# Kernel tuning notes

Measured on AMD Instinct MI355X. Metric: run time of the kernel, lower is better.

## Reference

```python
import jax, jax.numpy as jnp
import numpy as np

N, E = 50000, 800000
D_IN, D_HID, D_OUT = 128, 64, 32
NEG_SLOPE = 0.2


def _gat_layer(h_in, src, dst, W, a_s, a_d, b):
    # h_in: [N, din], W: [din, dout]
    h = h_in @ W                                   # [N, dout]
    alpha_src = h @ a_s                            # [N]
    alpha_dst = h @ a_d                            # [N]
    e = jax.nn.leaky_relu(alpha_src[src] + alpha_dst[dst], NEG_SLOPE)  # [E']
    # segment softmax over incoming edges of each dst node
    m = jax.ops.segment_max(e, dst, num_segments=N)
    ex = jnp.exp(e - m[dst])
    s = jax.ops.segment_sum(ex, dst, num_segments=N)
    w = ex / s[dst]                                # [E']
    out = jax.ops.segment_sum(h[src] * w[:, None], dst, num_segments=N)
    return out + b


def setup_inputs() -> dict:
    key = jax.random.key(0)
    ks = jax.random.split(key, 16)
    x = jax.random.normal(ks[0], (N, D_IN), dtype=jnp.float32)
    edge_index = jax.random.randint(ks[1], (2, E), 0, N, dtype=jnp.int64)
    dims = [(D_IN, D_HID), (D_HID, D_HID), (D_HID, D_OUT)]
    inp = {"x": x, "edge_index": edge_index}
    for i, (din, dout) in enumerate(dims):
        sc = 1.0 / np.sqrt(din)
        inp[f"W{i}"] = jax.random.normal(ks[2 + 4 * i], (din, dout), dtype=jnp.float32) * sc
        inp[f"as{i}"] = jax.random.normal(ks[3 + 4 * i], (dout,), dtype=jnp.float32) * 0.1
        inp[f"ad{i}"] = jax.random.normal(ks[4 + 4 * i], (dout,), dtype=jnp.float32) * 0.1
        inp[f"b{i}"] = jnp.zeros((dout,), dtype=jnp.float32)
    return inp


def reference(x, edge_index, W0, as0, ad0, b0, W1, as1, ad1, b1, W2, as2, ad2, b2):
    # add self loops (PyG GATConv default)
    loop = jnp.arange(N, dtype=edge_index.dtype)
    src = jnp.concatenate([edge_index[0], loop])
    dst = jnp.concatenate([edge_index[1], loop])
    h = jax.nn.relu(_gat_layer(x, src, dst, W0, as0, ad0, b0))
    h = jax.nn.relu(_gat_layer(h, src, dst, W1, as1, ad1, b1))
    h = jnp.tanh(_gat_layer(h, src, dst, W2, as2, ad2, b2))
    return h
```

## Files before the change

### kernel.cpp

```cpp
#include <hip/hip_runtime.h>
#include <hip/hip_fp16.h>
#include <math.h>

#define N_NODES 50000
#define E_EDGES 800000
#define ETOT    (E_EDGES + N_NODES)

#define BUCK_SHIFT 9
#define BUCK_SZ   (1 << BUCK_SHIFT)
#define NBUCK ((N_NODES + BUCK_SZ - 1) >> BUCK_SHIFT)
#define BS_EPT 16
#define BS_THREADS 256
#define BS_EPB (BS_THREADS * BS_EPT)
#define BS_NBLK ((ETOT + BS_EPB - 1) / BS_EPB)

template<int DIN, int DOUT>
__global__ __launch_bounds__(256)
void gemm_alpha_kernel(const float* __restrict__ X, const float* __restrict__ W,
                       const float* __restrict__ a_s, const float* __restrict__ a_d,
                       __half* __restrict__ H16, float* __restrict__ asrc,
                       float* __restrict__ adst)
{
    constexpr int COLG = DOUT / 4;
    constexpr int ROWG = 256 / COLG;
    constexpr int BM   = ROWG * 4;
    constexpr int K4   = DIN / 4;

    __shared__ float Xl[BM * DIN];
    __shared__ float Wl[DIN * DOUT];

    const int tid = threadIdx.x;
    const int row0b = blockIdx.x * BM;

    constexpr int WV = DIN * DOUT / 4;
    for (int i = tid; i < WV; i += 256)
        ((float4*)Wl)[i] = ((const float4*)W)[i];

    constexpr int XV = BM * K4;
    for (int i = tid; i < XV; i += 256) {
        int r  = i / K4;
        int j  = i % K4;
        int gr = row0b + r;
        float4 v = make_float4(0.f, 0.f, 0.f, 0.f);
        if (gr < N_NODES) v = ((const float4*)X)[gr * K4 + j];
        *(float4*)&Xl[r * DIN + ((j ^ ((r >> 2) & 7)) << 2)] = v;
    }
    __syncthreads();

    const int tx = tid % COLG;
    const int ty = tid / COLG;
    const int r0 = ty * 4;
    const int c0 = tx * 4;
    const int swz = ty & 7;

    float acc[4][4] = {};
    for (int kk = 0; kk < DIN; kk += 4) {
        float a[4][4], w[4][4];
        const int jk = ((kk >> 2) ^ swz) << 2;
#pragma unroll
        for (int i = 0; i < 4; ++i)
            *(float4*)a[i] = *(const float4*)&Xl[(r0 + i) * DIN + jk];
#pragma unroll
        for (int j = 0; j < 4; ++j)
            *(float4*)w[j] = *(const float4*)&Wl[(kk + j) * DOUT + c0];
#pragma unroll
        for (int i = 0; i < 4; ++i)
#pragma unroll
            for (int j = 0; j < 4; ++j)
                acc[i][j] = fmaf(a[i][0], w[0][j],
                            fmaf(a[i][1], w[1][j],
                            fmaf(a[i][2], w[2][j],
                            fmaf(a[i][3], w[3][j], acc[i][j]))));
    }

    float as4[4], ad4[4];
    *(float4*)as4 = *(const float4*)&a_s[c0];
    *(float4*)ad4 = *(const float4*)&a_d[c0];

#pragma unroll
    for (int i = 0; i < 4; ++i) {
        const int gr = row0b + r0 + i;
        float ps = acc[i][0] * as4[0] + acc[i][1] * as4[1] +
                   acc[i][2] * as4[2] + acc[i][3] * as4[3];
        float pd = acc[i][0] * ad4[0] + acc[i][1] * ad4[1] +
                   acc[i][2] * ad4[2] + acc[i][3] * ad4[3];
#pragma unroll
        for (int off = COLG / 2; off >= 1; off >>= 1) {
            ps += __shfl_xor(ps, off, 64);
            pd += __shfl_xor(pd, off, 64);
        }
        if (gr < N_NODES) {
            __half2 p01 = __floats2half2_rn(acc[i][0], acc[i][1]);
            __half2 p23 = __floats2half2_rn(acc[i][2], acc[i][3]);
            uint2 pk;
            pk.x = *(unsigned int*)&p01;
            pk.y = *(unsigned int*)&p23;
            *(uint2*)&H16[gr * DOUT + c0] = pk;
            if (tx == 0) { asrc[gr] = ps; adst[gr] = pd; }
        }
    }
}

__global__ __launch_bounds__(128)
void zero98_kernel(int* __restrict__ bcnt)
{
    int i = threadIdx.x;
    if (i < NBUCK) bcnt[i] = 0;
}

__global__ __launch_bounds__(BS_THREADS)
void hist_kernel(const int* __restrict__ ei, int* __restrict__ bcnt)
{
    __shared__ int lcnt[NBUCK];
    const int t = threadIdx.x;
    for (int i = t; i < NBUCK; i += BS_THREADS) lcnt[i] = 0;
    __syncthreads();
    const int e0 = blockIdx.x * BS_EPB;
#pragma unroll
    for (int k = 0; k < BS_EPT; ++k) {
        const int eid = e0 + k * BS_THREADS + t;
        if (eid < ETOT) {
            int dst = (eid < E_EDGES) ? ei[E_EDGES + eid] : (eid - E_EDGES);
            atomicAdd(&lcnt[dst >> BUCK_SHIFT], 1);
        }
    }
    __syncthreads();
    for (int i = t; i < NBUCK; i += BS_THREADS)
        if (lcnt[i] > 0) atomicAdd(&bcnt[i], lcnt[i]);
}

__global__ __launch_bounds__(128)
void scan98_kernel(const int* __restrict__ bcnt, int* __restrict__ cur,
                   int* __restrict__ cur0)
{
    __shared__ int lds[128];
    const int t = threadIdx.x;
    const int v = (t < NBUCK) ? bcnt[t] : 0;
    lds[t] = v;
    __syncthreads();
    for (int off = 1; off < 128; off <<= 1) {
        int u = (t >= off) ? lds[t - off] : 0;
        __syncthreads();
        lds[t] += u;
        __syncthreads();
    }
    if (t < NBUCK) { cur[t] = lds[t] - v; cur0[t] = lds[t] - v; }
}

__global__ __launch_bounds__(BS_THREADS)
void binscatter_kernel(const int* __restrict__ ei, int* __restrict__ cur,
                       unsigned int* __restrict__ tmp)
{
    __shared__ int lcnt[NBUCK];
    __shared__ int lbase[NBUCK];
    const int t = threadIdx.x;
    for (int i = t; i < NBUCK; i += BS_THREADS) lcnt[i] = 0;
    __syncthreads();

    const int e0 = blockIdx.x * BS_EPB;
    unsigned int pk[BS_EPT];
    int rk[BS_EPT];
    int bk[BS_EPT];
#pragma unroll
    for (int k = 0; k < BS_EPT; ++k) {
        const int eid = e0 + k * BS_THREADS + t;
        bk[k] = -1;
        if (eid < ETOT) {
            int src, dst;
            if (eid < E_EDGES) { src = ei[eid]; dst = ei[E_EDGES + eid]; }
            else               { src = dst = eid - E_EDGES; }
            bk[k] = dst >> BUCK_SHIFT;
            pk[k] = ((unsigned int)dst << 16) | (unsigned int)src;
            rk[k] = atomicAdd(&lcnt[bk[k]], 1);
        }
    }
    __syncthreads();
    for (int i = t; i < NBUCK; i += BS_THREADS)
        if (lcnt[i] > 0) lbase[i] = atomicAdd(&cur[i], lcnt[i]);
    __syncthreads();
#pragma unroll
    for (int k = 0; k < BS_EPT; ++k)
        if (bk[k] >= 0) tmp[lbase[bk[k]] + rk[k]] = pk[k];
}

__global__ __launch_bounds__(BUCK_SZ)
void bucket_sort_kernel(const unsigned int* __restrict__ tmp,
                        const int* __restrict__ cur0,
                        const int* __restrict__ bcnt,
                        unsigned int* __restrict__ csr_pk,
                        int* __restrict__ offs)
{
    __shared__ int lcnt[BUCK_SZ];
    __shared__ int loff[BUCK_SZ];
    __shared__ int lcur[BUCK_SZ];
    const int bk = blockIdx.x;
    const int t  = threadIdx.x;
    const int base = cur0[bk];
    const int cnt  = bcnt[bk];

    lcnt[t] = 0;
    __syncthreads();
    for (int i = t; i < cnt; i += BUCK_SZ)
        atomicAdd(&lcnt[(tmp[base + i] >> 16) & (BUCK_SZ - 1)], 1);
    __syncthreads();

    const int v = lcnt[t];
    loff[t] = v;
    __syncthreads();
    for (int off = 1; off < BUCK_SZ; off <<= 1) {
        int u = (t >= off) ? loff[t - off] : 0;
        __syncthreads();
        loff[t] += u;
        __syncthreads();
    }
    const int excl = loff[t] - v;

    const int g = (bk << BUCK_SHIFT) + t;
    if (g <= N_NODES) offs[g] = base + excl;

    lcur[t] = excl;
    __syncthreads();
    for (int i = t; i < cnt; i += BUCK_SZ) {
        const unsigned int pk = tmp[base + i];
        const int l = (pk >> 16) & (BUCK_SZ - 1);
        const int pos = atomicAdd(&lcur[l], 1);
        csr_pk[base + pos] = pk;
    }
}

template<int DOUT, int ACT>
__global__ __launch_bounds__(256)
void node_agg_kernel(const int* __restrict__ offs,
                     const unsigned int* __restrict__ csr_pk,
                     const float* __restrict__ asrc,
                     const float* __restrict__ adst,
                     const __half* __restrict__ H16,
                     const float* __restrict__ b,
                     float* __restrict__ out)
{
    constexpr int FL    = DOUT / 8;
    constexpr int SLOTS = 64 / FL;
    const int wv   = threadIdx.x >> 6;
    const int lane = threadIdx.x & 63;
    const int fl   = lane % FL;
    const int slot = lane / FL;
    const int node = blockIdx.x * 4 + wv;
    if (node >= N_NODES) return;

    const int beg = offs[node];
    const int end = offs[node + 1];
    const float adn = adst[node];
    const __half* __restrict__ Hf = H16 + fl * 8;

    float s = 0.f;
    float acc[8] = {};

    int eid = beg + slot;
    bool valid = (eid < end);
    unsigned int pk = valid ? csr_pk[eid] : 0u;

    for (int cb = beg; cb < end; cb += SLOTS) {
        const int nid = cb + SLOTS + slot;
        const bool nvalid = (nid < end);
        const unsigned int npk = nvalid ? csr_pk[nid] : 0u;

        float p = 0.f;
        uint4 h = make_uint4(0u, 0u, 0u, 0u);
        if (valid) {
            const unsigned int src = pk & 0xffffu;
            float v = asrc[src] + adn;
            v = fmaxf(v, 0.2f * v);
            p = __expf(fminf(v, 80.f));
            h = *(const uint4*)(Hf + src * DOUT);
        }
        const float2 f0 = __half22float2(*(const __half2*)&h.x);
        const float2 f1 = __half22float2(*(const __half2*)&h.y);
        const float2 f2 = __half22float2(*(const __half2*)&h.z);
        const float2 f3 = __half22float2(*(const __half2*)&h.w);
        s += p;
        acc[0] = fmaf(p, f0.x, acc[0]);
        acc[1] = fmaf(p, f0.y, acc[1]);
        acc[2] = fmaf(p, f1.x, acc[2]);
        acc[3] = fmaf(p, f1.y, acc[3]);
        acc[4] = fmaf(p, f2.x, acc[4]);
        acc[5] = fmaf(p, f2.y, acc[5]);
        acc[6] = fmaf(p, f3.x, acc[6]);
        acc[7] = fmaf(p, f3.y, acc[7]);
        valid = nvalid;
        pk = npk;
    }

#pragma unroll
    for (int off = FL; off < 64; off <<= 1) {
        s += __shfl_xor(s, off, 64);
#pragma unroll
        for (int j = 0; j < 8; ++j)
            acc[j] += __shfl_xor(acc[j], off, 64);
    }

    if (slot == 0) {
        const float inv = 1.f / s;
        float o[8];
#pragma unroll
        for (int j = 0; j < 8; ++j) {
            float v = acc[j] * inv + b[fl * 8 + j];
            o[j] = (ACT == 0) ? fmaxf(v, 0.f) : tanhf(v);
        }
        *(float4*)&out[node * DOUT + fl * 8]     = *(float4*)&o[0];
        *(float4*)&out[node * DOUT + fl * 8 + 4] = *(float4*)&o[4];
    }
}


template<int DIN, int DOUT, int ACT>
static void run_layer(const float* X, const float* W, const float* a_s,
                      const float* a_d, const float* b,
                      const int* offs, const unsigned int* csr_pk,
                      __half* H16, float* asrc, float* adst,
                      float* out, hipStream_t stream)
{
    constexpr int COLG = DOUT / 4;
    constexpr int BM = (256 / COLG) * 4;
    const int gemm_grid = (N_NODES + BM - 1) / BM;
    gemm_alpha_kernel<DIN, DOUT><<<gemm_grid, 256, 0, stream>>>(
        X, W, a_s, a_d, H16, asrc, adst);

    const int agg_grid = (N_NODES + 3) / 4;
    node_agg_kernel<DOUT, ACT><<<agg_grid, 256, 0, stream>>>(
        offs, csr_pk, asrc, adst, H16, b, out);
}

extern "C" void kernel_launch(void* const* d_in, const int* in_sizes, int n_in,
                              void* d_out, int out_size, void* d_ws, size_t ws_size,
                              hipStream_t stream)
{
    const float* x  = (const float*)d_in[0];
    const int*   ei = (const int*)d_in[1];
    const float* W0 = (const float*)d_in[2];
    const float* as0= (const float*)d_in[3];
    const float* ad0= (const float*)d_in[4];
    const float* b0 = (const float*)d_in[5];
    const float* W1 = (const float*)d_in[6];
    const float* as1= (const float*)d_in[7];
    const float* ad1= (const float*)d_in[8];
    const float* b1 = (const float*)d_in[9];
    const float* W2 = (const float*)d_in[10];
    const float* as2= (const float*)d_in[11];
    const float* ad2= (const float*)d_in[12];
    const float* b2 = (const float*)d_in[13];
    float* out = (float*)d_out;

    char* wsb = (char*)d_ws;
    auto take = [&](size_t bytes) {
        char* p = wsb;
        wsb += (bytes + 255) & ~size_t(255);
        return p;
    };
    __half* h16    = (__half*)take(sizeof(__half) * N_NODES * 64);
    float* buf_act = (float*)take(sizeof(float) * N_NODES * 64);
    float* asrc    = (float*)take(sizeof(float) * N_NODES);
    float* adst    = (float*)take(sizeof(float) * N_NODES);
    int*   offs    = (int*)take(sizeof(int) * (N_NODES + 1));
    int*   bcnt    = (int*)take(sizeof(int) * NBUCK);
    int*   cur     = (int*)take(sizeof(int) * NBUCK);
    int*   cur0    = (int*)take(sizeof(int) * NBUCK);
    unsigned int* csr_pk = (unsigned int*)take(sizeof(unsigned int) * ETOT);
    unsigned int* tmp = (unsigned int*)h16;

    zero98_kernel<<<1, 128, 0, stream>>>(bcnt);
    hist_kernel<<<BS_NBLK, BS_THREADS, 0, stream>>>(ei, bcnt);
    scan98_kernel<<<1, 128, 0, stream>>>(bcnt, cur, cur0);
    binscatter_kernel<<<BS_NBLK, BS_THREADS, 0, stream>>>(ei, cur, tmp);
    bucket_sort_kernel<<<NBUCK, BUCK_SZ, 0, stream>>>(tmp, cur0, bcnt,
                                                      csr_pk, offs);

    run_layer<128, 64, 0>(x, W0, as0, ad0, b0, offs, csr_pk,
                          h16, asrc, adst, buf_act, stream);
    run_layer<64, 64, 0>(buf_act, W1, as1, ad1, b1, offs, csr_pk,
                         h16, asrc, adst, buf_act, stream);
    run_layer<64, 32, 1>(buf_act, W2, as2, ad2, b2, offs, csr_pk,
                         h16, asrc, adst, out, stream);
}
```

Measured before the change: 184.6 us.

## Fuse histogram into first GEMM and aggregation into next-layer GEMM

Folds the destination-bucket histogram into the layer-0 GEMM kernel and replaces the zeroing kernel with a memset. Each layer's aggregation is fused with the following layer's GEMM and attention projection, so the activated hidden features stay in LDS and never travel through global memory as fp32. This drops several launches and the fp32 activation round trip. In exchange, the fused blocks process 64 nodes each with a fixed loop, giving fewer blocks and lower parallelism during the irregular aggregation phase, plus extra workspace for double-buffered features.

```diff
diff --git a/kernel.cpp b/kernel.cpp
--- a/kernel.cpp
+++ b/kernel.cpp
@@ -14,16 +14,19 @@
 #define BS_EPB (BS_THREADS * BS_EPT)
 #define BS_NBLK ((ETOT + BS_EPB - 1) / BS_EPB)
 
-template<int DIN, int DOUT>
+#define GEMM0_GRID ((N_NODES + 63) / 64)
+#define HPB ((ETOT + GEMM0_GRID - 1) / GEMM0_GRID)
+
 __global__ __launch_bounds__(256)
-void gemm_alpha_kernel(const float* __restrict__ X, const float* __restrict__ W,
+void gemm0_hist_kernel(const float* __restrict__ X, const float* __restrict__ W,
                        const float* __restrict__ a_s, const float* __restrict__ a_d,
+                       const int* __restrict__ ei, int* __restrict__ bcnt,
                        __half* __restrict__ H16, float* __restrict__ asrc,
                        float* __restrict__ adst)
 {
+    constexpr int DIN = 128, DOUT = 64;
     constexpr int COLG = DOUT / 4;
-    constexpr int ROWG = 256 / COLG;
-    constexpr int BM   = ROWG * 4;
+    constexpr int BM   = 64;
     constexpr int K4   = DIN / 4;
 
     __shared__ float Xl[BM * DIN];
@@ -32,12 +35,10 @@
     const int tid = threadIdx.x;
     const int row0b = blockIdx.x * BM;
 
-    constexpr int WV = DIN * DOUT / 4;
-    for (int i = tid; i < WV; i += 256)
+    for (int i = tid; i < DIN * DOUT / 4; i += 256)
         ((float4*)Wl)[i] = ((const float4*)W)[i];
 
-    constexpr int XV = BM * K4;
-    for (int i = tid; i < XV; i += 256) {
+    for (int i = tid; i < BM * K4; i += 256) {
         int r  = i / K4;
         int j  = i % K4;
         int gr = row0b + r;
@@ -99,34 +100,20 @@
             if (tx == 0) { asrc[gr] = ps; adst[gr] = pd; }
         }
     }
-}
-
-__global__ __launch_bounds__(128)
-void zero98_kernel(int* __restrict__ bcnt)
-{
-    int i = threadIdx.x;
-    if (i < NBUCK) bcnt[i] = 0;
-}
-
-__global__ __launch_bounds__(BS_THREADS)
-void hist_kernel(const int* __restrict__ ei, int* __restrict__ bcnt)
-{
-    __shared__ int lcnt[NBUCK];
-    const int t = threadIdx.x;
-    for (int i = t; i < NBUCK; i += BS_THREADS) lcnt[i] = 0;
-    __syncthreads();
-    const int e0 = blockIdx.x * BS_EPB;
-#pragma unroll
-    for (int k = 0; k < BS_EPT; ++k) {
-        const int eid = e0 + k * BS_THREADS + t;
-        if (eid < ETOT) {
-            int dst = (eid < E_EDGES) ? ei[E_EDGES + eid] : (eid - E_EDGES);
-            atomicAdd(&lcnt[dst >> BUCK_SHIFT], 1);
-        }
-    }
-    __syncthreads();
-    for (int i = t; i < NBUCK; i += BS_THREADS)
-        if (lcnt[i] > 0) atomicAdd(&bcnt[i], lcnt[i]);
+
+    __syncthreads();
+    int* lh = (int*)Xl;
+    for (int i = tid; i < NBUCK; i += 256) lh[i] = 0;
+    __syncthreads();
+    const int h0 = blockIdx.x * HPB;
+    const int hend = min(h0 + HPB, ETOT);
+    for (int eid = h0 + tid; eid < hend; eid += 256) {
+        int dst = (eid < E_EDGES) ? ei[E_EDGES + eid] : (eid - E_EDGES);
+        atomicAdd(&lh[dst >> BUCK_SHIFT], 1);
+    }
+    __syncthreads();
+    for (int i = tid; i < NBUCK; i += 256)
+        if (lh[i] > 0) atomicAdd(&bcnt[i], lh[i]);
 }
 
 __global__ __launch_bounds__(128)
@@ -225,6 +212,163 @@
         const int l = (pk >> 16) & (BUCK_SZ - 1);
         const int pos = atomicAdd(&lcur[l], 1);
         csr_pk[base + pos] = pk;
+    }
+}
+
+template<int DOUT>
+__global__ __launch_bounds__(256)
+void fused_agg_gemm_kernel(const int* __restrict__ offs,
+                           const unsigned int* __restrict__ csr_pk,
+                           const float* __restrict__ asrc_p,
+                           const float* __restrict__ adst_p,
+                           const __half* __restrict__ H16_p,
+                           const float* __restrict__ b_p,
+                           const float* __restrict__ W,
+                           const float* __restrict__ a_s,
+                           const float* __restrict__ a_d,
+                           __half* __restrict__ H16_n,
+                           float* __restrict__ asrc_n,
+                           float* __restrict__ adst_n)
+{
+    constexpr int DIN = 64;
+    constexpr int BM  = 64;
+    __shared__ float Xl[BM * DIN];
+    __shared__ float Wl[DIN * DOUT];
+
+    const int tid = threadIdx.x;
+    for (int i = tid; i < DIN * DOUT / 4; i += 256)
+        ((float4*)Wl)[i] = ((const float4*)W)[i];
+
+    const int wv   = tid >> 6;
+    const int lane = tid & 63;
+    const int fl   = lane & 7;
+    const int slot = lane >> 3;
+    const int node0 = blockIdx.x * BM;
+    const __half* __restrict__ Hf = H16_p + fl * 8;
+
+    for (int it = 0; it < 16; ++it) {
+        const int r = it * 4 + wv;
+        const int node = node0 + r;
+        float s = 0.f;
+        float acc[8] = {};
+        if (node < N_NODES) {
+            const int beg = offs[node];
+            const int end = offs[node + 1];
+            const float adn = adst_p[node];
+            int eid = beg + slot;
+            bool valid = (eid < end);
+            unsigned int pk = valid ? csr_pk[eid] : 0u;
+            for (int cb = beg; cb < end; cb += 8) {
+                const int nid = cb + 8 + slot;
+                const bool nvalid = (nid < end);
+                const unsigned int npk = nvalid ? csr_pk[nid] : 0u;
+                float p = 0.f;
+                uint4 h = make_uint4(0u, 0u, 0u, 0u);
+                if (valid) {
+                    const unsigned int src = pk & 0xffffu;
+                    float v = asrc_p[src] + adn;
+                    v = fmaxf(v, 0.2f * v);
+                    p = __expf(fminf(v, 80.f));
+                    h = *(const uint4*)(Hf + src * 64);
+                }
+                const float2 f0 = __half22float2(*(const __half2*)&h.x);
+                const float2 f1 = __half22float2(*(const __half2*)&h.y);
+                const float2 f2 = __half22float2(*(const __half2*)&h.z);
+                const float2 f3 = __half22float2(*(const __half2*)&h.w);
+                s += p;
+                acc[0] = fmaf(p, f0.x, acc[0]);
+                acc[1] = fmaf(p, f0.y, acc[1]);
+                acc[2] = fmaf(p, f1.x, acc[2]);
+                acc[3] = fmaf(p, f1.y, acc[3]);
+                acc[4] = fmaf(p, f2.x, acc[4]);
+                acc[5] = fmaf(p, f2.y, acc[5]);
+                acc[6] = fmaf(p, f3.x, acc[6]);
+                acc[7] = fmaf(p, f3.y, acc[7]);
+                valid = nvalid;
+                pk = npk;
+            }
+        }
+#pragma unroll
+        for (int off = 8; off < 64; off <<= 1) {
+            s += __shfl_xor(s, off, 64);
+#pragma unroll
+            for (int j = 0; j < 8; ++j)
+                acc[j] += __shfl_xor(acc[j], off, 64);
+        }
+        if (slot == 0) {
+            float o[8];
+            if (node < N_NODES) {
+                const float inv = 1.f / s;
+#pragma unroll
+                for (int j = 0; j < 8; ++j)
+                    o[j] = fmaxf(acc[j] * inv + b_p[fl * 8 + j], 0.f);
+            } else {
+#pragma unroll
+                for (int j = 0; j < 8; ++j) o[j] = 0.f;
+            }
+            const int sw = (r >> 2) & 7;
+            *(float4*)&Xl[r * DIN + (((fl * 2) ^ sw) << 2)] =
+                make_float4(o[0], o[1], o[2], o[3]);
+            *(float4*)&Xl[r * DIN + (((fl * 2 + 1) ^ sw) << 2)] =
+                make_float4(o[4], o[5], o[6], o[7]);
+        }
+    }
+    __syncthreads();
+
+    constexpr int COLG = DOUT / 4;
+    constexpr int ROWG = 256 / COLG;
+    constexpr int RPT  = BM / ROWG;
+    const int tx = tid % COLG;
+    const int ty = tid / COLG;
+    const int r0 = ty * RPT;
+    const int c0 = tx * 4;
+    const int swz = (r0 >> 2) & 7;
+
+    float acg[RPT][4] = {};
+    for (int kk = 0; kk < DIN; kk += 4) {
+        float a[RPT][4], w[4][4];
+        const int jk = ((kk >> 2) ^ swz) << 2;
+#pragma unroll
+        for (int i = 0; i < RPT; ++i)
+            *(float4*)a[i] = *(const float4*)&Xl[(r0 + i) * DIN + jk];
+#pragma unroll
+        for (int j = 0; j < 4; ++j)
+            *(float4*)w[j] = *(const float4*)&Wl[(kk + j) * DOUT + c0];
+#pragma unroll
+        for (int i = 0; i < RPT; ++i)
+#pragma unroll
+            for (int j = 0; j < 4; ++j)
+                acg[i][j] = fmaf(a[i][0], w[0][j],
+                            fmaf(a[i][1], w[1][j],
+                            fmaf(a[i][2], w[2][j],
+                            fmaf(a[i][3], w[3][j], acg[i][j]))));
+    }
+
+    float as4[4], ad4[4];
+    *(float4*)as4 = *(const float4*)&a_s[c0];
+    *(float4*)ad4 = *(const float4*)&a_d[c0];
+
+#pragma unroll
+    for (int i = 0; i < RPT; ++i) {
+        const int gr = node0 + r0 + i;
+        float ps = acg[i][0] * as4[0] + acg[i][1] * as4[1] +
+                   acg[i][2] * as4[2] + acg[i][3] * as4[3];
+        float pd = acg[i][0] * ad4[0] + acg[i][1] * ad4[1] +
+                   acg[i][2] * ad4[2] + acg[i][3] * ad4[3];
+#pragma unroll
+        for (int off = COLG / 2; off >= 1; off >>= 1) {
+            ps += __shfl_xor(ps, off, 64);
+            pd += __shfl_xor(pd, off, 64);
+        }
+        if (gr < N_NODES) {
+            __half2 p01 = __floats2half2_rn(acg[i][0], acg[i][1]);
+            __half2 p23 = __floats2half2_rn(acg[i][2], acg[i][3]);
+            uint2 pk;
+            pk.x = *(unsigned int*)&p01;
+            pk.y = *(unsigned int*)&p23;
+            *(uint2*)&H16_n[gr * DOUT + c0] = pk;
+            if (tx == 0) { asrc_n[gr] = ps; adst_n[gr] = pd; }
+        }
     }
 }
 
@@ -312,24 +456,6 @@
 }
 
 
-template<int DIN, int DOUT, int ACT>
-static void run_layer(const float* X, const float* W, const float* a_s,
-                      const float* a_d, const float* b,
-                      const int* offs, const unsigned int* csr_pk,
-                      __half* H16, float* asrc, float* adst,
-                      float* out, hipStream_t stream)
-{
-    constexpr int COLG = DOUT / 4;
-    constexpr int BM = (256 / COLG) * 4;
-    const int gemm_grid = (N_NODES + BM - 1) / BM;
-    gemm_alpha_kernel<DIN, DOUT><<<gemm_grid, 256, 0, stream>>>(
-        X, W, a_s, a_d, H16, asrc, adst);
-
-    const int agg_grid = (N_NODES + 3) / 4;
-    node_agg_kernel<DOUT, ACT><<<agg_grid, 256, 0, stream>>>(
-        offs, csr_pk, asrc, adst, H16, b, out);
-}
-
 extern "C" void kernel_launch(void* const* d_in, const int* in_sizes, int n_in,
                               void* d_out, int out_size, void* d_ws, size_t ws_size,
                               hipStream_t stream)
@@ -356,28 +482,38 @@
         wsb += (bytes + 255) & ~size_t(255);
         return p;
     };
-    __half* h16    = (__half*)take(sizeof(__half) * N_NODES * 64);
-    float* buf_act = (float*)take(sizeof(float) * N_NODES * 64);
-    float* asrc    = (float*)take(sizeof(float) * N_NODES);
-    float* adst    = (float*)take(sizeof(float) * N_NODES);
+    __half* h16a   = (__half*)take(sizeof(__half) * N_NODES * 64);
+    __half* h16b   = (__half*)take(sizeof(__half) * N_NODES * 64);
+    float* asrc_a  = (float*)take(sizeof(float) * N_NODES);
+    float* adst_a  = (float*)take(sizeof(float) * N_NODES);
+    float* asrc_b  = (float*)take(sizeof(float) * N_NODES);
+    float* adst_b  = (float*)take(sizeof(float) * N_NODES);
     int*   offs    = (int*)take(sizeof(int) * (N_NODES + 1));
     int*   bcnt    = (int*)take(sizeof(int) * NBUCK);
     int*   cur     = (int*)take(sizeof(int) * NBUCK);
     int*   cur0    = (int*)take(sizeof(int) * NBUCK);
+    unsigned int* tmp    = (unsigned int*)take(sizeof(unsigned int) * ETOT);
     unsigned int* csr_pk = (unsigned int*)take(sizeof(unsigned int) * ETOT);
-    unsigned int* tmp = (unsigned int*)h16;
-
-    zero98_kernel<<<1, 128, 0, stream>>>(bcnt);
-    hist_kernel<<<BS_NBLK, BS_THREADS, 0, stream>>>(ei, bcnt);
+
+    hipMemsetAsync(bcnt, 0, sizeof(int) * NBUCK, stream);
+
+    gemm0_hist_kernel<<<GEMM0_GRID, 256, 0, stream>>>(
+        x, W0, as0, ad0, ei, bcnt, h16a, asrc_a, adst_a);
+
     scan98_kernel<<<1, 128, 0, stream>>>(bcnt, cur, cur0);
     binscatter_kernel<<<BS_NBLK, BS_THREADS, 0, stream>>>(ei, cur, tmp);
     bucket_sort_kernel<<<NBUCK, BUCK_SZ, 0, stream>>>(tmp, cur0, bcnt,
                                                       csr_pk, offs);
 
-    run_layer<128, 64, 0>(x, W0, as0, ad0, b0, offs, csr_pk,
-                          h16, asrc, adst, buf_act, stream);
-    run_layer<64, 64, 0>(buf_act, W1, as1, ad1, b1, offs, csr_pk,
-                         h16, asrc, adst, buf_act, stream);
-    run_layer<64, 32, 1>(buf_act, W2, as2, ad2, b2, offs, csr_pk,
-                         h16, asrc, adst, out, stream);
-}
+    fused_agg_gemm_kernel<64><<<GEMM0_GRID, 256, 0, stream>>>(
+        offs, csr_pk, asrc_a, adst_a, h16a, b0,
+        W1, as1, ad1, h16b, asrc_b, adst_b);
+
+    fused_agg_gemm_kernel<32><<<GEMM0_GRID, 256, 0, stream>>>(
+        offs, csr_pk, asrc_b, adst_b, h16b, b1,
+        W2, as2, ad2, h16a, asrc_a, adst_a);
+
+    const int agg_grid = (N_NODES + 3) / 4;
+    node_agg_kernel<32, 1><<<agg_grid, 256, 0, stream>>>(
+        offs, csr_pk, asrc_a, adst_a, h16a, b2, out);
+}
```

New measurement: 315.5 us. +71.0%, slower.

## Fuse edge histogram into layer-0 GEMM and fold bucket scans into consumers

Applied to the files above, without the earlier changes.

The destination-bucket histogram moves into the first-layer GEMM kernel as a tail phase, so the GEMM and histogram share one launch. The separate zero and scan kernels are removed: counters are cleared with a memset, and both binscatter and bucket_sort now recompute the prefix scan of bucket counts locally. The temporary sort buffer gets its own workspace instead of aliasing h16, since h16 is now written before the sort. This cuts kernel launches and serialization at the cost of redundant per-block scans and an extra buffer.

```diff
diff --git a/kernel.cpp b/kernel.cpp
--- a/kernel.cpp
+++ b/kernel.cpp
@@ -14,16 +14,19 @@
 #define BS_EPB (BS_THREADS * BS_EPT)
 #define BS_NBLK ((ETOT + BS_EPB - 1) / BS_EPB)
 
-template<int DIN, int DOUT>
+#define GEMM0_GRID ((N_NODES + 63) / 64)
+#define HPB ((ETOT + GEMM0_GRID - 1) / GEMM0_GRID)
+
 __global__ __launch_bounds__(256)
-void gemm_alpha_kernel(const float* __restrict__ X, const float* __restrict__ W,
+void gemm0_hist_kernel(const float* __restrict__ X, const float* __restrict__ W,
                        const float* __restrict__ a_s, const float* __restrict__ a_d,
+                       const int* __restrict__ ei, int* __restrict__ bcnt,
                        __half* __restrict__ H16, float* __restrict__ asrc,
                        float* __restrict__ adst)
 {
+    constexpr int DIN = 128, DOUT = 64;
     constexpr int COLG = DOUT / 4;
-    constexpr int ROWG = 256 / COLG;
-    constexpr int BM   = ROWG * 4;
+    constexpr int BM   = 64;
     constexpr int K4   = DIN / 4;
 
     __shared__ float Xl[BM * DIN];
@@ -32,12 +35,10 @@
     const int tid = threadIdx.x;
     const int row0b = blockIdx.x * BM;
 
-    constexpr int WV = DIN * DOUT / 4;
-    for (int i = tid; i < WV; i += 256)
+    for (int i = tid; i < DIN * DOUT / 4; i += 256)
         ((float4*)Wl)[i] = ((const float4*)W)[i];
 
-    constexpr int XV = BM * K4;
-    for (int i = tid; i < XV; i += 256) {
+    for (int i = tid; i < BM * K4; i += 256) {
         int r  = i / K4;
         int j  = i % K4;
         int gr = row0b + r;
@@ -99,61 +100,131 @@
             if (tx == 0) { asrc[gr] = ps; adst[gr] = pd; }
         }
     }
-}
-
-__global__ __launch_bounds__(128)
-void zero98_kernel(int* __restrict__ bcnt)
-{
-    int i = threadIdx.x;
-    if (i < NBUCK) bcnt[i] = 0;
+
+    __syncthreads();
+    int* lh = (int*)Xl;
+    for (int i = tid; i < NBUCK; i += 256) lh[i] = 0;
+    __syncthreads();
+    const int h0 = blockIdx.x * HPB;
+    const int hend = min(h0 + HPB, ETOT);
+    for (int eid = h0 + tid; eid < hend; eid += 256) {
+        int dst = (eid < E_EDGES) ? ei[E_EDGES + eid] : (eid - E_EDGES);
+        atomicAdd(&lh[dst >> BUCK_SHIFT], 1);
+    }
+    __syncthreads();
+    for (int i = tid; i < NBUCK; i += 256)
+        if (lh[i] > 0) atomicAdd(&bcnt[i], lh[i]);
+}
+
+template<int DIN, int DOUT>
+__global__ __launch_bounds__(256)
+void gemm_alpha_kernel(const float* __restrict__ X, const float* __restrict__ W,
+                       const float* __restrict__ a_s, const float* __restrict__ a_d,
+                       __half* __restrict__ H16, float* __restrict__ asrc,
+                       float* __restrict__ adst)
+{
+    constexpr int COLG = DOUT / 4;
+    constexpr int ROWG = 256 / COLG;
+    constexpr int BM   = ROWG * 4;
+    constexpr int K4   = DIN / 4;
+
+    __shared__ float Xl[BM * DIN];
+    __shared__ float Wl[DIN * DOUT];
+
+    const int tid = threadIdx.x;
+    const int row0b = blockIdx.x * BM;
+
+    for (int i = tid; i < DIN * DOUT / 4; i += 256)
+        ((float4*)Wl)[i] = ((const float4*)W)[i];
+
+    for (int i = tid; i < BM * K4; i += 256) {
+        int r  = i / K4;
+        int j  = i % K4;
+        int gr = row0b + r;
+        float4 v = make_float4(0.f, 0.f, 0.f, 0.f);
+        if (gr < N_NODES) v = ((const float4*)X)[gr * K4 + j];
+        *(float4*)&Xl[r * DIN + ((j ^ ((r >> 2) & 7)) << 2)] = v;
+    }
+    __syncthreads();
+
+    const int tx = tid % COLG;
+    const int ty = tid / COLG;
+    const int r0 = ty * 4;
+    const int c0 = tx * 4;
+    const int swz = ty & 7;
+
+    float acc[4][4] = {};
+    for (int kk = 0; kk < DIN; kk += 4) {
+        float a[4][4], w[4][4];
+        const int jk = ((kk >> 2) ^ swz) << 2;
+#pragma unroll
+        for (int i = 0; i < 4; ++i)
+            *(float4*)a[i] = *(const float4*)&Xl[(r0 + i) * DIN + jk];
+#pragma unroll
+        for (int j = 0; j < 4; ++j)
+            *(float4*)w[j] = *(const float4*)&Wl[(kk + j) * DOUT + c0];
+#pragma unroll
+        for (int i = 0; i < 4; ++i)
+#pragma unroll
+            for (int j = 0; j < 4; ++j)
+                acc[i][j] = fmaf(a[i][0], w[0][j],
+                            fmaf(a[i][1], w[1][j],
+                            fmaf(a[i][2], w[2][j],
+                            fmaf(a[i][3], w[3][j], acc[i][j]))));
+    }
+
+    float as4[4], ad4[4];
+    *(float4*)as4 = *(const float4*)&a_s[c0];
+    *(float4*)ad4 = *(const float4*)&a_d[c0];
+
+#pragma unroll
+    for (int i = 0; i < 4; ++i) {
+        const int gr = row0b + r0 + i;
+        float ps = acc[i][0] * as4[0] + acc[i][1] * as4[1] +
+                   acc[i][2] * as4[2] + acc[i][3] * as4[3];
+        float pd = acc[i][0] * ad4[0] + acc[i][1] * ad4[1] +
+                   acc[i][2] * ad4[2] + acc[i][3] * ad4[3];
+#pragma unroll
+        for (int off = COLG / 2; off >= 1; off >>= 1) {
+            ps += __shfl_xor(ps, off, 64);
+            pd += __shfl_xor(pd, off, 64);
+        }
+        if (gr < N_NODES) {
+            __half2 p01 = __floats2half2_rn(acc[i][0], acc[i][1]);
+            __half2 p23 = __floats2half2_rn(acc[i][2], acc[i][3]);
+            uint2 pk;
+            pk.x = *(unsigned int*)&p01;
+            pk.y = *(unsigned int*)&p23;
+            *(uint2*)&H16[gr * DOUT + c0] = pk;
+            if (tx == 0) { asrc[gr] = ps; adst[gr] = pd; }
+        }
+    }
 }
 
 __global__ __launch_bounds__(BS_THREADS)
-void hist_kernel(const int* __restrict__ ei, int* __restrict__ bcnt)
-{
-    __shared__ int lcnt[NBUCK];
-    const int t = threadIdx.x;
-    for (int i = t; i < NBUCK; i += BS_THREADS) lcnt[i] = 0;
-    __syncthreads();
-    const int e0 = blockIdx.x * BS_EPB;
-#pragma unroll
-    for (int k = 0; k < BS_EPT; ++k) {
-        const int eid = e0 + k * BS_THREADS + t;
-        if (eid < ETOT) {
-            int dst = (eid < E_EDGES) ? ei[E_EDGES + eid] : (eid - E_EDGES);
-            atomicAdd(&lcnt[dst >> BUCK_SHIFT], 1);
-        }
-    }
-    __syncthreads();
-    for (int i = t; i < NBUCK; i += BS_THREADS)
-        if (lcnt[i] > 0) atomicAdd(&bcnt[i], lcnt[i]);
-}
-
-__global__ __launch_bounds__(128)
-void scan98_kernel(const int* __restrict__ bcnt, int* __restrict__ cur,
-                   int* __restrict__ cur0)
-{
-    __shared__ int lds[128];
-    const int t = threadIdx.x;
-    const int v = (t < NBUCK) ? bcnt[t] : 0;
-    lds[t] = v;
-    __syncthreads();
-    for (int off = 1; off < 128; off <<= 1) {
-        int u = (t >= off) ? lds[t - off] : 0;
-        __syncthreads();
-        lds[t] += u;
-        __syncthreads();
-    }
-    if (t < NBUCK) { cur[t] = lds[t] - v; cur0[t] = lds[t] - v; }
-}
-
-__global__ __launch_bounds__(BS_THREADS)
-void binscatter_kernel(const int* __restrict__ ei, int* __restrict__ cur,
-                       unsigned int* __restrict__ tmp)
+void binscatter_kernel(const int* __restrict__ ei, const int* __restrict__ bcnt,
+                       int* __restrict__ cur, unsigned int* __restrict__ tmp)
 {
     __shared__ int lcnt[NBUCK];
     __shared__ int lbase[NBUCK];
+    __shared__ int lscan[128];
     const int t = threadIdx.x;
+
+    if (t < 128) {
+        const int v = (t < NBUCK) ? bcnt[t] : 0;
+        lscan[t] = v;
+        __syncthreads();
+        for (int off = 1; off < 128; off <<= 1) {
+            int u = (t >= off) ? lscan[t - off] : 0;
+            __syncthreads();
+            lscan[t] += u;
+            __syncthreads();
+        }
+        if (t < NBUCK) lbase[t] = lscan[t] - v;
+    } else {
+        __syncthreads();
+        for (int off = 1; off < 128; off <<= 1) { __syncthreads(); __syncthreads(); }
+    }
     for (int i = t; i < NBUCK; i += BS_THREADS) lcnt[i] = 0;
     __syncthreads();
 
@@ -176,7 +247,7 @@
     }
     __syncthreads();
     for (int i = t; i < NBUCK; i += BS_THREADS)
-        if (lcnt[i] > 0) lbase[i] = atomicAdd(&cur[i], lcnt[i]);
+        if (lcnt[i] > 0) lbase[i] += atomicAdd(&cur[i], lcnt[i]);
     __syncthreads();
 #pragma unroll
     for (int k = 0; k < BS_EPT; ++k)
@@ -185,7 +256,6 @@
 
 __global__ __launch_bounds__(BUCK_SZ)
 void bucket_sort_kernel(const unsigned int* __restrict__ tmp,
-                        const int* __restrict__ cur0,
                         const int* __restrict__ bcnt,
                         unsigned int* __restrict__ csr_pk,
                         int* __restrict__ offs)
@@ -193,9 +263,24 @@
     __shared__ int lcnt[BUCK_SZ];
     __shared__ int loff[BUCK_SZ];
     __shared__ int lcur[BUCK_SZ];
+    __shared__ int sbase;
     const int bk = blockIdx.x;
     const int t  = threadIdx.x;
-    const int base = cur0[bk];
+
+    {
+        const int v = (t < NBUCK) ? bcnt[t] : 0;
+        lcnt[t] = v;
+        __syncthreads();
+        for (int off = 1; off < 128; off <<= 1) {
+            int u = (t >= off && t < 128) ? lcnt[t - off] : 0;
+            __syncthreads();
+            if (t < 128) lcnt[t] += u;
+            __syncthreads();
+        }
+        if (t == bk) sbase = lcnt[t] - v;
+    }
+    __syncthreads();
+    const int base = sbase;
     const int cnt  = bcnt[bk];
 
     lcnt[t] = 0;
@@ -312,24 +397,6 @@
 }
 
 
-template<int DIN, int DOUT, int ACT>
-static void run_layer(const float* X, const float* W, const float* a_s,
-                      const float* a_d, const float* b,
-                      const int* offs, const unsigned int* csr_pk,
-                      __half* H16, float* asrc, float* adst,
-                      float* out, hipStream_t stream)
-{
-    constexpr int COLG = DOUT / 4;
-    constexpr int BM = (256 / COLG) * 4;
-    const int gemm_grid = (N_NODES + BM - 1) / BM;
-    gemm_alpha_kernel<DIN, DOUT><<<gemm_grid, 256, 0, stream>>>(
-        X, W, a_s, a_d, H16, asrc, adst);
-
-    const int agg_grid = (N_NODES + 3) / 4;
-    node_agg_kernel<DOUT, ACT><<<agg_grid, 256, 0, stream>>>(
-        offs, csr_pk, asrc, adst, H16, b, out);
-}
-
 extern "C" void kernel_launch(void* const* d_in, const int* in_sizes, int n_in,
                               void* d_out, int out_size, void* d_ws, size_t ws_size,
                               hipStream_t stream)
@@ -361,23 +428,31 @@
     float* asrc    = (float*)take(sizeof(float) * N_NODES);
     float* adst    = (float*)take(sizeof(float) * N_NODES);
     int*   offs    = (int*)take(sizeof(int) * (N_NODES + 1));
-    int*   bcnt    = (int*)take(sizeof(int) * NBUCK);
-    int*   cur     = (int*)take(sizeof(int) * NBUCK);
-    int*   cur0    = (int*)take(sizeof(int) * NBUCK);
+    int*   bc      = (int*)take(sizeof(int) * NBUCK * 2);
+    int*   bcnt    = bc;
+    int*   cur     = bc + NBUCK;
+    unsigned int* tmp    = (unsigned int*)take(sizeof(unsigned int) * ETOT);
     unsigned int* csr_pk = (unsigned int*)take(sizeof(unsigned int) * ETOT);
-    unsigned int* tmp = (unsigned int*)h16;
-
-    zero98_kernel<<<1, 128, 0, stream>>>(bcnt);
-    hist_kernel<<<BS_NBLK, BS_THREADS, 0, stream>>>(ei, bcnt);
-    scan98_kernel<<<1, 128, 0, stream>>>(bcnt, cur, cur0);
-    binscatter_kernel<<<BS_NBLK, BS_THREADS, 0, stream>>>(ei, cur, tmp);
-    bucket_sort_kernel<<<NBUCK, BUCK_SZ, 0, stream>>>(tmp, cur0, bcnt,
-                                                      csr_pk, offs);
-
-    run_layer<128, 64, 0>(x, W0, as0, ad0, b0, offs, csr_pk,
-                          h16, asrc, adst, buf_act, stream);
-    run_layer<64, 64, 0>(buf_act, W1, as1, ad1, b1, offs, csr_pk,
-                         h16, asrc, adst, buf_act, stream);
-    run_layer<64, 32, 1>(buf_act, W2, as2, ad2, b2, offs, csr_pk,
-                         h16, asrc, adst, out, stream);
-}
+
+    hipMemsetAsync(bc, 0, sizeof(int) * NBUCK * 2, stream);
+
+    gemm0_hist_kernel<<<GEMM0_GRID, 256, 0, stream>>>(
+        x, W0, as0, ad0, ei, bcnt, h16, asrc, adst);
+
+    binscatter_kernel<<<BS_NBLK, BS_THREADS, 0, stream>>>(ei, bcnt, cur, tmp);
+    bucket_sort_kernel<<<NBUCK, BUCK_SZ, 0, stream>>>(tmp, bcnt, csr_pk, offs);
+
+    const int agg_grid = (N_NODES + 3) / 4;
+    node_agg_kernel<64, 0><<<agg_grid, 256, 0, stream>>>(
+        offs, csr_pk, asrc, adst, h16, b0, buf_act);
+
+    gemm_alpha_kernel<64, 64><<<GEMM0_GRID, 256, 0, stream>>>(
+        buf_act, W1, as1, ad1, h16, asrc, adst);
+    node_agg_kernel<64, 0><<<agg_grid, 256, 0, stream>>>(
+        offs, csr_pk, asrc, adst, h16, b1, buf_act);
+
+    gemm_alpha_kernel<64, 32><<<(N_NODES + 127) / 128, 256, 0, stream>>>(
+        buf_act, W2, as2, ad2, h16, asrc, adst);
+    node_agg_kernel<32, 1><<<agg_grid, 256, 0, stream>>>(
+        offs, csr_pk, asrc, adst, h16, b2, out);
+}
```

Measured after the change: 186.5 us. Within noise of the previous version (+1.0%).
